# Kernel optimization log

Hardware: AMD Instinct MI355X
Metric: run time of the kernel (lower is better)

Reference implementation:

```python
import jax, jax.numpy as jnp
import numpy as np

B, C, H, W = 8, 1, 256, 256
ALPHA, GAMMA = 0.25, 2.0
DICE_W, BOUNDARY_W, FOCAL_W = 1.0, 0.5, 1.0
EPS = 1e-06


def _dt1d(f, axis):
    # exact 1D squared-distance transform: out[i] = min_j (i-j)^2 + f[j]
    n = f.shape[axis]
    f = jnp.moveaxis(f, axis, -1)
    i = jnp.arange(n)
    D = ((i[:, None] - i[None, :]) ** 2).astype(f.dtype)  # [n, n]
    out = jnp.min(f[..., None, :] + D, axis=-1)
    return jnp.moveaxis(out, -1, axis)


def edt(mask):
    # Euclidean distance from nonzero elements to nearest zero element,
    # computed over ALL axes (matches scipy.distance_transform_edt on the 4D array).
    inf = jnp.asarray(float(sum(n * n for n in mask.shape) + 1), jnp.float32)
    f = jnp.where(mask, inf, jnp.float32(0.0))
    for ax in range(mask.ndim):  # structural loop over 4 axes
        f = _dt1d(f, ax)
    return jnp.sqrt(f)


def setup_inputs() -> dict:
    key = jax.random.key(0)
    k1, k2 = jax.random.split(key)
    logits = jax.random.normal(k1, (B, C, H, W), dtype=jnp.float32)
    targets = jax.random.uniform(k2, (B, C, H, W), dtype=jnp.float32)
    return {"logits": logits, "targets": targets}


def reference(logits, targets):
    p = jax.nn.sigmoid(logits)

    # Dice loss
    inter = jnp.sum(p * targets)
    dice = 1.0 - (2.0 * inter + EPS) / (jnp.sum(p) + jnp.sum(targets) + EPS)

    # Boundary loss (distance transform over the full 4D mask)
    dm = edt(targets > 0.5)
    boundary = jnp.mean(dm * (1.0 - p) ** 2)

    # Focal loss (stable BCE with logits)
    ce = jnp.maximum(logits, 0.0) - logits * targets + jnp.log1p(jnp.exp(-jnp.abs(logits)))
    p_t = p * targets + (1.0 - p) * (1.0 - targets)
    focal = jnp.mean(ALPHA * (1.0 - p_t) ** GAMMA * ce)

    return DICE_W * dice + BOUNDARY_W * boundary + FOCAL_W * focal
```

## Files before the change

kernel.cpp:

```cpp
#include <hip/hip_runtime.h>
#include <math.h>

namespace {

constexpr int Bn = 8;
constexpr int Hn = 256;
constexpr int Wn = 256;
constexpr int HW = Hn * Wn;
constexpr int Ntot = Bn * HW;
constexpr float INF_F = 131138.0f;
constexpr float EPSv = 1e-6f;

__device__ __forceinline__ float blkred(float v, float* sm) {
    #pragma unroll
    for (int o = 32; o > 0; o >>= 1) v += __shfl_down(v, o, 64);
    int lane = threadIdx.x & 63, wid = threadIdx.x >> 6;
    __syncthreads();
    if (lane == 0) sm[wid] = v;
    __syncthreads();
    return sm[0] + sm[1] + sm[2] + sm[3];
}

__device__ __forceinline__ float dt_thread(const float* __restrict__ u, int i) {
    const float4* u4 = reinterpret_cast<const float4*>(u);
    float ni2 = -2.0f * (float)i;
    float mA = 3.0e38f, mB = 3.0e38f;
    float jb = 0.f;
    #pragma unroll 8
    for (int q = 0; q < 64; ++q) {
        float4 uu = u4[q];
        mA = fminf(fminf(mA, fmaf(ni2, jb, uu.x)),
                   fmaf(ni2, jb + 1.f, uu.y));
        mB = fminf(fminf(mB, fmaf(ni2, jb + 2.f, uu.z)),
                   fmaf(ni2, jb + 3.f, uu.w));
        jb += 4.f;
    }
    return fminf(mA, mB) + (float)i * (float)i;
}

__global__ __launch_bounds__(256) void kAW(const float* __restrict__ lg,
                                           const float* __restrict__ tg,
                                           float* __restrict__ gT,
                                           float* __restrict__ pa) {
    int blk = blockIdx.x;
    int b = blk >> 8, h = blk & 255;
    int w = threadIdx.x;
    int t = h * Wn + w;
    float x = lg[(size_t)b * HW + t];
    float tv = 0.f;
    float m = 3.0e38f;
    #pragma unroll
    for (int j = 0; j < Bn; ++j) {
        float tj = tg[(size_t)j * HW + t];
        if (j == b) tv = tj;
        float fv = (tj > 0.5f) ? INF_F : 0.f;
        int d = b - j;
        m = fminf(m, fv + (float)(d * d));
    }
    float p  = 1.f / (1.f + expf(-x));
    float sp = p, st = tv, spt = p * tv;
    float ce = fmaxf(x, 0.f) - x * tv + log1pf(expf(-fabsf(x)));
    float pt = p * tv + (1.f - p) * (1.f - tv);
    float om = 1.f - pt;
    float fo = 0.25f * om * om * ce;

    __shared__ __align__(16) float u[Wn];
    __shared__ float sm[4];
    u[w] = m + (float)w * (float)w;
    __syncthreads();
    float res = dt_thread(u, w);
    gT[((size_t)b * Wn + w) * Hn + h] = res;

    sp  = blkred(sp, sm);
    st  = blkred(st, sm);
    spt = blkred(spt, sm);
    fo  = blkred(fo, sm);
    if (threadIdx.x == 0) {
        float* o = pa + blk * 4;
        o[0] = sp; o[1] = st; o[2] = spt; o[3] = fo;
    }
}

__global__ __launch_bounds__(256) void kH(const float* __restrict__ gT,
                                          const float* __restrict__ lg,
                                          float* __restrict__ bp) {
    int blk = blockIdx.x;
    int b = blk >> 8, w = blk & 255;
    int i = threadIdx.x;
    __shared__ __align__(16) float u[Hn];
    __shared__ float sm[4];
    u[i] = gT[(size_t)blk * Hn + i] + (float)i * (float)i;
    float x = lg[(size_t)b * HW + i * Wn + w];
    __syncthreads();
    float res = dt_thread(u, i);
    float s = 1.f / (1.f + expf(x));
    float acc = sqrtf(res) * s * s;
    acc = blkred(acc, sm);
    if (i == 0) bp[blk] = acc;
}

__global__ __launch_bounds__(256) void kD(const float* __restrict__ pa,
                                          const float* __restrict__ bp,
                                          float* __restrict__ out) {
    __shared__ float sm[4];
    int t = threadIdx.x;
    float sp = 0.f, st = 0.f, spt = 0.f, fo = 0.f, bs = 0.f;
    #pragma unroll
    for (int k = 0; k < 8; ++k) {
        const float* o = pa + (size_t)(t + 256 * k) * 4;
        sp += o[0]; st += o[1]; spt += o[2]; fo += o[3];
        bs += bp[t + 256 * k];
    }
    sp  = blkred(sp, sm);
    st  = blkred(st, sm);
    spt = blkred(spt, sm);
    fo  = blkred(fo, sm);
    bs  = blkred(bs, sm);
    if (t == 0) {
        float dice = 1.f - (2.f * spt + EPSv) / (sp + st + EPSv);
        float boundary = bs / (float)Ntot;
        float focal = fo / (float)Ntot;
        out[0] = 1.0f * dice + 0.5f * boundary + 1.0f * focal;
    }
}

}

extern "C" void kernel_launch(void* const* d_in, const int* in_sizes, int n_in,
                              void* d_out, int out_size, void* d_ws, size_t ws_size,
                              hipStream_t stream) {
    const float* lg = (const float*)d_in[0];
    const float* tg = (const float*)d_in[1];
    float* ws = (float*)d_ws;
    float* gT = ws;
    float* pa = ws + Ntot;
    float* bp = ws + Ntot + 8192;

    kAW<<<Bn * Hn, 256, 0, stream>>>(lg, tg, gT, pa);
    kH<<<Bn * Wn, 256, 0, stream>>>(gT, lg, bp);
    kD<<<1, 256, 0, stream>>>(pa, bp, (float*)d_out);
}
```

Baseline: 29.95 us.

## Process four rows per block with register-blocked 1D distance transform

Each block now handles four image rows, one wavefront per row. Every lane computes four output columns, so each shared-memory float4 read is reused across four distance minima, and inputs are loaded as float4. The transposed store to the intermediate buffer is staged through shared memory so each thread writes a float4 of four consecutive rows. This cuts the block count and LDS traffic per output, in exchange for more registers per thread and fewer blocks in flight.

Measured after the change: 30.02 us. Within noise of the previous version (+0.2%).

```diff
diff --git a/kernel.cpp b/kernel.cpp
--- a/kernel.cpp
+++ b/kernel.cpp
@@ -8,6 +8,8 @@
 constexpr int Wn = 256;
 constexpr int HW = Hn * Wn;
 constexpr int Ntot = Bn * HW;
+constexpr int NAW = Bn * 64;
+constexpr int NBH = Bn * Wn;
 constexpr float INF_F = 131138.0f;
 constexpr float EPSv = 1e-6f;
 
@@ -19,6 +21,39 @@
     if (lane == 0) sm[wid] = v;
     __syncthreads();
     return sm[0] + sm[1] + sm[2] + sm[3];
+}
+
+__device__ __forceinline__ float getc(const float4& v, int r) {
+    return r == 0 ? v.x : r == 1 ? v.y : r == 2 ? v.z : v.w;
+}
+
+__device__ __forceinline__ void dt_wave4(const float* __restrict__ u,
+                                         int lane, float res[4]) {
+    const float4* u4 = reinterpret_cast<const float4*>(u);
+    float fi[4], ni2[4], mA[4], mB[4];
+    #pragma unroll
+    for (int r = 0; r < 4; ++r) {
+        fi[r]  = (float)(4 * lane + r);
+        ni2[r] = -2.0f * fi[r];
+        mA[r] = 3.0e38f; mB[r] = 3.0e38f;
+    }
+    float jb = 0.f;
+    #pragma unroll 8
+    for (int q = 0; q < 64; ++q) {
+        float4 uu = u4[q];
+        float j0 = jb, j1 = jb + 1.f, j2 = jb + 2.f, j3 = jb + 3.f;
+        jb += 4.f;
+        #pragma unroll
+        for (int r = 0; r < 4; ++r) {
+            mA[r] = fminf(fminf(mA[r], fmaf(ni2[r], j0, uu.x)),
+                          fmaf(ni2[r], j1, uu.y));
+            mB[r] = fminf(fminf(mB[r], fmaf(ni2[r], j2, uu.z)),
+                          fmaf(ni2[r], j3, uu.w));
+        }
+    }
+    #pragma unroll
+    for (int r = 0; r < 4; ++r)
+        res[r] = fminf(mA[r], mB[r]) + fi[r] * fi[r];
 }
 
 __device__ __forceinline__ float dt_thread(const float* __restrict__ u, int i) {
@@ -42,43 +77,63 @@
                                            const float* __restrict__ tg,
                                            float* __restrict__ gT,
                                            float* __restrict__ pa) {
+    __shared__ __align__(16) float uL[4][Wn];
+    __shared__ __align__(16) float vL[4][Wn];
+    __shared__ float sm[4];
+    int tid = threadIdx.x, wv = tid >> 6, lane = tid & 63;
     int blk = blockIdx.x;
-    int b = blk >> 8, h = blk & 255;
-    int w = threadIdx.x;
-    int t = h * Wn + w;
-    float x = lg[(size_t)b * HW + t];
-    float tv = 0.f;
-    float m = 3.0e38f;
+    int b = blk >> 6;
+    int h0 = (blk & 63) * 4;
+    int h = h0 + wv;
+    int w4 = lane * 4;
+
+    float4 xg = *reinterpret_cast<const float4*>(lg + (size_t)b * HW + h * Wn + w4);
+    float4 tgv[Bn];
     #pragma unroll
-    for (int j = 0; j < Bn; ++j) {
-        float tj = tg[(size_t)j * HW + t];
-        if (j == b) tv = tj;
-        float fv = (tj > 0.5f) ? INF_F : 0.f;
-        int d = b - j;
-        m = fminf(m, fv + (float)(d * d));
+    for (int j = 0; j < Bn; ++j)
+        tgv[j] = *reinterpret_cast<const float4*>(tg + (size_t)j * HW + h * Wn + w4);
+    float d2[Bn];
+    #pragma unroll
+    for (int j = 0; j < Bn; ++j) { int e = b - j; d2[j] = (float)(e * e); }
+
+    float sp = 0.f, st = 0.f, spt = 0.f, fo = 0.f;
+    float uv[4];
+    #pragma unroll
+    for (int r = 0; r < 4; ++r) {
+        float x  = getc(xg, r);
+        float tv = getc(tgv[b], r);
+        float p  = 1.f / (1.f + expf(-x));
+        sp  += p;
+        st  += tv;
+        spt += p * tv;
+        float ce = fmaxf(x, 0.f) - x * tv + log1pf(expf(-fabsf(x)));
+        float pt = p * tv + (1.f - p) * (1.f - tv);
+        float om = 1.f - pt;
+        fo += 0.25f * om * om * ce;
+        float m = 3.0e38f;
+        #pragma unroll
+        for (int j = 0; j < Bn; ++j) {
+            float fv = getc(tgv[j], r) > 0.5f ? INF_F : 0.f;
+            m = fminf(m, fv + d2[j]);
+        }
+        float wF = (float)(w4 + r);
+        uv[r] = m + wF * wF;
     }
-    float p  = 1.f / (1.f + expf(-x));
-    float sp = p, st = tv, spt = p * tv;
-    float ce = fmaxf(x, 0.f) - x * tv + log1pf(expf(-fabsf(x)));
-    float pt = p * tv + (1.f - p) * (1.f - tv);
-    float om = 1.f - pt;
-    float fo = 0.25f * om * om * ce;
-
-    __shared__ __align__(16) float u[Wn];
-    __shared__ float sm[4];
-    u[w] = m + (float)w * (float)w;
-    __syncthreads();
-    float res = dt_thread(u, w);
-    gT[((size_t)b * Wn + w) * Hn + h] = res;
+    *reinterpret_cast<float4*>(&uL[wv][w4]) = make_float4(uv[0], uv[1], uv[2], uv[3]);
+    float res[4];
+    dt_wave4(uL[wv], lane, res);
+    *reinterpret_cast<float4*>(&vL[wv][w4]) = make_float4(res[0], res[1], res[2], res[3]);
 
     sp  = blkred(sp, sm);
     st  = blkred(st, sm);
     spt = blkred(spt, sm);
     fo  = blkred(fo, sm);
-    if (threadIdx.x == 0) {
+    if (tid == 0) {
         float* o = pa + blk * 4;
         o[0] = sp; o[1] = st; o[2] = spt; o[3] = fo;
     }
+    float4 gv = make_float4(vL[0][tid], vL[1][tid], vL[2][tid], vL[3][tid]);
+    *reinterpret_cast<float4*>(gT + ((size_t)b * Wn + tid) * Hn + h0) = gv;
 }
 
 __global__ __launch_bounds__(256) void kH(const float* __restrict__ gT,
@@ -106,11 +161,12 @@
     int t = threadIdx.x;
     float sp = 0.f, st = 0.f, spt = 0.f, fo = 0.f, bs = 0.f;
     #pragma unroll
-    for (int k = 0; k < 8; ++k) {
+    for (int k = 0; k < 2; ++k) {
         const float* o = pa + (size_t)(t + 256 * k) * 4;
         sp += o[0]; st += o[1]; spt += o[2]; fo += o[3];
-        bs += bp[t + 256 * k];
     }
+    #pragma unroll
+    for (int k = 0; k < 8; ++k) bs += bp[t + 256 * k];
     sp  = blkred(sp, sm);
     st  = blkred(st, sm);
     spt = blkred(spt, sm);
@@ -134,9 +190,9 @@
     float* ws = (float*)d_ws;
     float* gT = ws;
     float* pa = ws + Ntot;
-    float* bp = ws + Ntot + 8192;
+    float* bp = ws + Ntot + 4 * NAW;
 
-    kAW<<<Bn * Hn, 256, 0, stream>>>(lg, tg, gT, pa);
-    kH<<<Bn * Wn, 256, 0, stream>>>(gT, lg, bp);
+    kAW<<<NAW, 256, 0, stream>>>(lg, tg, gT, pa);
+    kH<<<NBH, 256, 0, stream>>>(gT, lg, bp);
     kD<<<1, 256, 0, stream>>>(pa, bp, (float*)d_out);
 }
```
